# Optimization experiments

Measured on AMD Instinct MI355X. Metric: run time of the kernel, lower is better.

The kernel has to match this reference:

```python
import jax, jax.numpy as jnp
import numpy as np

B, P, D, H, A, C = 256, 512, 16, 256, 8, 2
HID = 256
IN_MLP = H + A + 1  # 265


def setup_inputs() -> dict:
    key = jax.random.key(0)
    ks = jax.random.split(key, 12)
    s = 0.05  # small init for recurrent stability
    return {
        "particles": jax.random.normal(ks[0], (B, P, D), jnp.float32),
        "weights": jax.random.uniform(ks[1], (B, P), jnp.float32),
        "actions": jax.random.normal(ks[2], (B, A), jnp.float32),
        "time": jax.random.uniform(ks[3], (B,), jnp.float32) * 100.0,
        "Wi": jax.random.normal(ks[4], (D + 1, 3 * H), jnp.float32) * s,
        "bi": jnp.zeros((3 * H,), jnp.float32),
        "Wh_rz": jax.random.normal(ks[5], (H, 2 * H), jnp.float32) * s,
        "Wh_n": jax.random.normal(ks[6], (H, H), jnp.float32) * s,
        "bn": jnp.zeros((H,), jnp.float32),
        "mlp_W1": jax.random.normal(ks[7], (C, IN_MLP, HID), jnp.float32) * s,
        "mlp_b1": jnp.zeros((C, HID), jnp.float32),
        "mlp_W2": jax.random.normal(ks[8], (C, HID, HID), jnp.float32) * s,
        "mlp_b2": jnp.zeros((C, HID), jnp.float32),
        "mlp_W3": jax.random.normal(ks[9], (C, HID, 1), jnp.float32) * s,
        "mlp_b3": jnp.zeros((C, 1), jnp.float32),
        "num_time_steps": 100,
    }


def reference(particles, weights, actions, time, Wi, bi, Wh_rz, Wh_n, bn,
              mlp_W1, mlp_b1, mlp_W2, mlp_b2, mlp_W3, mlp_b3, num_time_steps):
    # feature_fn = identity; append weights as an extra feature channel
    x = jnp.concatenate([particles, weights[..., None]], axis=-1)  # [B, P, D+1]
    xs = jnp.swapaxes(x, 0, 1)  # [P, B, D+1], scan over particle axis

    def gru_step(h, xt):
        gi = xt @ Wi + bi  # [B, 3H]
        i_r, i_z, i_n = jnp.split(gi, 3, axis=-1)
        hrz = h @ Wh_rz  # [B, 2H], no bias (flax GRUCell hidden r/z dense)
        r = jax.nn.sigmoid(i_r + hrz[:, :H])
        z = jax.nn.sigmoid(i_z + hrz[:, H:])
        n = jnp.tanh(i_n + r * (h @ Wh_n + bn))
        h_new = (1.0 - z) * n + z * h
        return h_new, None

    h0 = jnp.zeros((particles.shape[0], H), particles.dtype)
    enc, _ = jax.lax.scan(gru_step, h0, xs)  # last hidden == take(outputs, -1, axis=-2)

    norm_time = time / num_time_steps
    hidden = jnp.concatenate([enc, actions, norm_time[..., None]], axis=-1)  # [B, IN_MLP]

    # n_critics MLPs evaluated batched over critic axis c
    h1 = jax.nn.relu(jnp.einsum('bi,cio->bco', hidden, mlp_W1) + mlp_b1)
    h2 = jax.nn.relu(jnp.einsum('bci,cio->bco', h1, mlp_W2) + mlp_b2)
    q = jnp.einsum('bci,cio->bco', h2, mlp_W3) + mlp_b3  # [B, C, 1]
    return q[..., 0]  # [B, C]
```

## Files before the change

kernel.cpp:

```cpp
#include <hip/hip_runtime.h>
#include <hip/hip_fp16.h>

typedef _Float16 h2v __attribute__((ext_vector_type(2)));
typedef _Float16 f16x8 __attribute__((ext_vector_type(8)));
typedef float f32x4 __attribute__((ext_vector_type(4)));
typedef unsigned int u32;
typedef unsigned short u16;

#define NB 256
#define NP 512
#define NH 256

#define OFF_WH 0
#define LEN_WH 98304
#define OFF_WIB (OFF_WH + LEN_WH)
#define LEN_WIB 12288
#define OFF_W1 (OFF_WIB + LEN_WIB)
#define LEN_W1 68096
#define OFF_W2 (OFF_W1 + LEN_W1)
#define LEN_W2 65536
#define OFF_W3 (OFF_W2 + LEN_W2)
#define LEN_W3 256
#define WS_DWORDS (OFF_W3 + LEN_W3)

__device__ __forceinline__ u32 pack2(float lo, float hi) {
    h2v v; v.x = (_Float16)lo; v.y = (_Float16)hi;
    return __builtin_bit_cast(u32, v);
}

__device__ __forceinline__ float fdot2(u32 a, u32 b, float c) {
#if __has_builtin(__builtin_amdgcn_fdot2)
    return __builtin_amdgcn_fdot2(__builtin_bit_cast(h2v, a),
                                  __builtin_bit_cast(h2v, b), c, false);
#else
    h2v x = __builtin_bit_cast(h2v, a), y = __builtin_bit_cast(h2v, b);
    return c + (float)x.x * (float)y.x + (float)x.y * (float)y.y;
#endif
}

__global__ __launch_bounds__(256) void pack_kernel(
    const float* __restrict__ Wi, const float* __restrict__ Whrz,
    const float* __restrict__ Whn, const float* __restrict__ W1,
    const float* __restrict__ W2, const float* __restrict__ W3,
    u32* __restrict__ ws)
{
    for (int F = blockIdx.x * 256 + threadIdx.x; F < WS_DWORDS; F += gridDim.x * 256) {
        u32 val;
        if (F < OFF_WIB) {
            int d = F & 3; int r = F >> 2;
            int l = r & 63; int q = r >> 6;
            int f = q % 48; int w = q / 48;
            int t = f >> 3; int kt = f & 7;
            int g = t >> 1, c = t & 1;
            int k = kt * 32 + ((l >> 4) << 3) + 2 * d;
            int col = g * 256 + w * 32 + c * 16 + (l & 15);
            float lo, hi;
            if (col < 512) { lo = Whrz[k * 512 + col]; hi = Whrz[(k + 1) * 512 + col]; }
            else { lo = Whn[k * 256 + (col - 512)]; hi = Whn[(k + 1) * 256 + (col - 512)]; }
            val = pack2(lo, hi);
        } else if (F < OFF_W1) {
            int j = F - OFF_WIB;
            int d = j & 3; int r = j >> 2;
            int l = r & 63; int q = r >> 6;
            int t = q % 6; int w = q / 6;
            int g = t >> 1, c = t & 1;
            int k = ((l >> 4) << 3) + 2 * d;
            int col = g * 256 + w * 32 + c * 16 + (l & 15);
            float lo = (k < 17) ? Wi[k * 768 + col] : 0.f;
            float hi = (k + 1 < 17) ? Wi[(k + 1) * 768 + col] : 0.f;
            val = pack2(lo, hi);
        } else if (F < OFF_W2) {
            int j = F - OFF_W1; int c = j / (133 * 256); int r = j % (133 * 256);
            int kk = r >> 8; int o = r & 255;
            int k = 2 * kk;
            float lo = W1[(c * 265 + k) * 256 + o];
            float hi = (k + 1 < 265) ? W1[(c * 265 + k + 1) * 256 + o] : 0.f;
            val = pack2(lo, hi);
        } else if (F < OFF_W3) {
            int j = F - OFF_W2; int c = j >> 15; int r = j & 32767;
            int kk = r >> 8; int o = r & 255;
            float lo = W2[(c * 256 + 2 * kk) * 256 + o];
            float hi = W2[(c * 256 + 2 * kk + 1) * 256 + o];
            val = pack2(lo, hi);
        } else {
            int j = F - OFF_W3; int c = j >> 7; int jj = j & 127;
            float lo = W3[c * 256 + 2 * jj];
            float hi = W3[c * 256 + 2 * jj + 1];
            val = pack2(lo, hi);
        }
        ws[F] = val;
    }
}

__global__ __launch_bounds__(512, 2) void qnet_kernel(
    const float* __restrict__ particles, const float* __restrict__ pweights,
    const float* __restrict__ actions, const float* __restrict__ timev,
    const float* __restrict__ bi, const float* __restrict__ bn,
    const float* __restrict__ b1, const float* __restrict__ b2,
    const float* __restrict__ b3, const int* __restrict__ nts,
    const u32* __restrict__ ws, float* __restrict__ out)
{
    __shared__ __align__(16) u32 sX[NP * 16];
    __shared__ __align__(16) float sG[8 * 1536];
    __shared__ __align__(16) u32 sH2[2][128];
    __shared__ __align__(16) float sHf[NH];
    __shared__ __align__(16) float sMisc[16];

    const int b = blockIdx.x;
    const int tid = threadIdx.x;
    const int lane = tid & 63;
    const int wid = tid >> 6;

    f16x8 bfh[48];
    {
        const uint4* gp = (const uint4*)(ws + OFF_WH) + (wid * 48) * 64 + lane;
        #pragma unroll
        for (int i = 0; i < 48; ++i) bfh[i] = __builtin_bit_cast(f16x8, gp[i * 64]);
    }
    {
        const float2* pr2 = (const float2*)(particles + (long)b * NP * 16);
        for (int j = tid; j < NP * 8; j += 512) {
            int p = j >> 3, q = j & 7;
            float2 v = pr2[j];
            sX[p * 16 + q] = pack2(v.x, v.y);
        }
        const float* wr = pweights + (long)b * NP;
        for (int j = tid; j < NP * 8; j += 512) {
            int p = j >> 3, q = j & 7;
            sX[p * 16 + 8 + q] = (q == 0) ? pack2(wr[p], 0.f) : 0u;
        }
    }
    if (tid < 256) ((u32*)sH2)[tid] = 0u;
    if (tid < 8) sMisc[tid] = actions[b * 8 + tid];
    if (tid == 8) sMisc[8] = timev[b] / (float)nts[0];

    float birL = 0.f, bizL = 0.f, binnL = 0.f, bnnL = 0.f, hreg = 0.f;
    if (lane < 32) {
        int j = wid * 32 + lane;
        birL = bi[j]; bizL = bi[NH + j]; binnL = bi[2 * NH + j]; bnnL = bn[j];
    }
    __syncthreads();

    const uint4* wibp = (const uint4*)(ws + OFF_WIB) + (wid * 6) * 64 + lane;

    #pragma unroll 1
    for (int p = 0; p < NP; ++p) {
        if ((p & 15) == 0) {
            f16x8 av = __builtin_bit_cast(f16x8,
                ((const uint4*)sX)[(p + (lane & 15)) * 4 + (lane >> 4)]);
            f32x4 z4 = {0.f, 0.f, 0.f, 0.f};
            f32x4 g0 = __builtin_amdgcn_mfma_f32_16x16x32_f16(av, __builtin_bit_cast(f16x8, wibp[0 * 64]), z4, 0, 0, 0);
            f32x4 g1 = __builtin_amdgcn_mfma_f32_16x16x32_f16(av, __builtin_bit_cast(f16x8, wibp[1 * 64]), z4, 0, 0, 0);
            f32x4 g2 = __builtin_amdgcn_mfma_f32_16x16x32_f16(av, __builtin_bit_cast(f16x8, wibp[2 * 64]), z4, 0, 0, 0);
            f32x4 g3 = __builtin_amdgcn_mfma_f32_16x16x32_f16(av, __builtin_bit_cast(f16x8, wibp[3 * 64]), z4, 0, 0, 0);
            f32x4 g4 = __builtin_amdgcn_mfma_f32_16x16x32_f16(av, __builtin_bit_cast(f16x8, wibp[4 * 64]), z4, 0, 0, 0);
            f32x4 g5 = __builtin_amdgcn_mfma_f32_16x16x32_f16(av, __builtin_bit_cast(f16x8, wibp[5 * 64]), z4, 0, 0, 0);
            int sb = (lane >> 4) << 2;
            float* gw = sG + wid * 1536 + (lane & 15);
            #pragma unroll
            for (int r = 0; r < 4; ++r) {
                gw[(sb + r) * 32]          = g0[r];
                gw[(sb + r) * 32 + 16]     = g1[r];
                gw[512 + (sb + r) * 32]    = g2[r];
                gw[512 + (sb + r) * 32 + 16] = g3[r];
                gw[1024 + (sb + r) * 32]   = g4[r];
                gw[1024 + (sb + r) * 32 + 16] = g5[r];
            }
            __syncthreads();
        }

        float gR = 0.f, gZ = 0.f, gN = 0.f;
        {
            const float* gp = sG + wid * 1536 + (p & 15) * 32 + (lane & 31);
            gR = gp[0]; gZ = gp[512]; gN = gp[1024];
        }

        const u32* hbuf = sH2[p & 1];
        f32x4 a0 = {0.f, 0.f, 0.f, 0.f}, a1 = a0, a2 = a0, a3 = a0, a4 = a0, a5 = a0;
        #pragma unroll
        for (int kt = 0; kt < 8; ++kt) {
            f16x8 hv = __builtin_bit_cast(f16x8, ((const uint4*)hbuf)[kt * 4 + (lane >> 4)]);
            a0 = __builtin_amdgcn_mfma_f32_16x16x32_f16(hv, bfh[kt],      a0, 0, 0, 0);
            a1 = __builtin_amdgcn_mfma_f32_16x16x32_f16(hv, bfh[8 + kt],  a1, 0, 0, 0);
            a2 = __builtin_amdgcn_mfma_f32_16x16x32_f16(hv, bfh[16 + kt], a2, 0, 0, 0);
            a3 = __builtin_amdgcn_mfma_f32_16x16x32_f16(hv, bfh[24 + kt], a3, 0, 0, 0);
            a4 = __builtin_amdgcn_mfma_f32_16x16x32_f16(hv, bfh[32 + kt], a4, 0, 0, 0);
            a5 = __builtin_amdgcn_mfma_f32_16x16x32_f16(hv, bfh[40 + kt], a5, 0, 0, 0);
        }

        bool hic = (lane & 16) != 0;
        float srm = hic ? a1[0] : a0[0];
        float szm = hic ? a3[0] : a2[0];
        float snm = hic ? a5[0] : a4[0];
        if (lane < 32) {
            float xr = gR + birL + srm;
            float xz = gZ + bizL + szm;
            float xn = gN + binnL;
            float r = 1.f / (1.f + __expf(-xr));
            float z = 1.f / (1.f + __expf(-xz));
            float targ = xn + r * (snm + bnnL);
            float e2 = __expf(2.f * targ);
            float n = 1.f - 2.f / (e2 + 1.f);
            hreg = (1.f - z) * n + z * hreg;
            _Float16 hh = (_Float16)hreg;
            ((u16*)sH2[(p + 1) & 1])[wid * 32 + lane] = __builtin_bit_cast(u16, hh);
        }
        __syncthreads();
    }

    if (lane < 32) sHf[wid * 32 + lane] = hreg;
    __syncthreads();
    u32* sHid = (u32*)sG;
    u16* sL1 = (u16*)(sG + 512);
    u16* sL2 = (u16*)(sG + 1024);
    if (tid < 128) sHid[tid] = pack2(sHf[2 * tid], sHf[2 * tid + 1]);
    else if (tid < 132) { int i = tid - 128; sHid[tid] = pack2(sMisc[2 * i], sMisc[2 * i + 1]); }
    else if (tid == 132) sHid[132] = pack2(sMisc[8], 0.f);
    __syncthreads();
    {
        int c = tid >> 8, o = tid & 255;
        float acc = b1[c * 256 + o];
        const u32* wp = ws + OFF_W1 + c * 133 * 256 + o;
        #pragma unroll 4
        for (int kk = 0; kk < 133; ++kk) acc = fdot2(wp[kk * 256], sHid[kk], acc);
        acc = fmaxf(acc, 0.f);
        _Float16 a16 = (_Float16)acc;
        sL1[tid] = __builtin_bit_cast(u16, a16);
    }
    __syncthreads();
    {
        int c = tid >> 8, o = tid & 255;
        float acc = b2[c * 256 + o];
        const u32* wp = ws + OFF_W2 + c * 128 * 256 + o;
        const u32* hp = (const u32*)sL1 + c * 128;
        #pragma unroll 4
        for (int kk = 0; kk < 128; ++kk) acc = fdot2(wp[kk * 256], hp[kk], acc);
        acc = fmaxf(acc, 0.f);
        _Float16 a16 = (_Float16)acc;
        sL2[tid] = __builtin_bit_cast(u16, a16);
    }
    __syncthreads();
    if (tid < 128) {
        int c = tid >> 6, l = tid & 63;
        const u32* wp = ws + OFF_W3 + c * 128;
        const u32* hp = (const u32*)sL2 + c * 128;
        float acc = fdot2(wp[l], hp[l], 0.f);
        acc = fdot2(wp[64 + l], hp[64 + l], acc);
        #pragma unroll
        for (int off = 32; off > 0; off >>= 1) acc += __shfl_down(acc, off);
        if (l == 0) out[b * 2 + c] = acc + b3[c];
    }
}

extern "C" void kernel_launch(void* const* d_in, const int* in_sizes, int n_in,
                              void* d_out, int out_size, void* d_ws, size_t ws_size,
                              hipStream_t stream) {
    const float* particles = (const float*)d_in[0];
    const float* pweights  = (const float*)d_in[1];
    const float* actions   = (const float*)d_in[2];
    const float* timev     = (const float*)d_in[3];
    const float* Wi        = (const float*)d_in[4];
    const float* bi        = (const float*)d_in[5];
    const float* Whrz      = (const float*)d_in[6];
    const float* Whn       = (const float*)d_in[7];
    const float* bn        = (const float*)d_in[8];
    const float* W1        = (const float*)d_in[9];
    const float* b1        = (const float*)d_in[10];
    const float* W2        = (const float*)d_in[11];
    const float* b2        = (const float*)d_in[12];
    const float* W3        = (const float*)d_in[13];
    const float* b3        = (const float*)d_in[14];
    const int*   nts       = (const int*)d_in[15];
    u32* ws = (u32*)d_ws;
    float* outp = (float*)d_out;

    pack_kernel<<<(WS_DWORDS + 255) / 256, 256, 0, stream>>>(Wi, Whrz, Whn, W1, W2, W3, ws);
    qnet_kernel<<<NB, 512, 0, stream>>>(particles, pweights, actions, timev,
                                        bi, bn, b1, b2, b3, nts, ws, outp);
}
```

Measured before the change: 629.6 us.

## Replace per-step MFMA recurrent matvec with packed fp16 dot2 on register-held weights

The recurrent h·Wh product per particle step used MFMA with a 16-row batch where only one row was meaningful, wasting most of the matrix work. It now uses v_dot2 fp16 instructions: each lane holds 192 packed weight pairs for one output column and half of K, and the two halves are reduced with a cross-lane shuffle. The pack kernel is rewritten to produce the new weight layout. This removes the wasted MFMA work but adds more scalar VALU instructions, a shuffle and broadcast LDS reads of h, and raises register pressure to 192 weight registers per lane under launch bounds of 512 threads and 2 blocks, which may cause spills.

Result: slower. 742.9 us (+18.0%).

```diff
diff --git a/kernel.cpp b/kernel.cpp
--- a/kernel.cpp
+++ b/kernel.cpp
@@ -47,13 +47,11 @@
     for (int F = blockIdx.x * 256 + threadIdx.x; F < WS_DWORDS; F += gridDim.x * 256) {
         u32 val;
         if (F < OFF_WIB) {
-            int d = F & 3; int r = F >> 2;
-            int l = r & 63; int q = r >> 6;
-            int f = q % 48; int w = q / 48;
-            int t = f >> 3; int kt = f & 7;
-            int g = t >> 1, c = t & 1;
-            int k = kt * 32 + ((l >> 4) << 3) + 2 * d;
-            int col = g * 256 + w * 32 + c * 16 + (l & 15);
+            int l = F & 63; int t = F >> 6;
+            int i = t % 192; int w = t / 192;
+            int g = i >> 6; int tt = i & 63;
+            int col = g * 256 + w * 32 + (l & 31);
+            int k = ((l >> 5) << 7) + 2 * tt;
             float lo, hi;
             if (col < 512) { lo = Whrz[k * 512 + col]; hi = Whrz[(k + 1) * 512 + col]; }
             else { lo = Whn[k * 256 + (col - 512)]; hi = Whn[(k + 1) * 256 + (col - 512)]; }
@@ -102,7 +100,7 @@
 {
     __shared__ __align__(16) u32 sX[NP * 16];
     __shared__ __align__(16) float sG[8 * 1536];
-    __shared__ __align__(16) u32 sH2[2][128];
+    __shared__ __align__(16) u16 sH2[2][NH];
     __shared__ __align__(16) float sHf[NH];
     __shared__ __align__(16) float sMisc[16];
 
@@ -111,11 +109,11 @@
     const int lane = tid & 63;
     const int wid = tid >> 6;
 
-    f16x8 bfh[48];
-    {
-        const uint4* gp = (const uint4*)(ws + OFF_WH) + (wid * 48) * 64 + lane;
+    u32 wreg[192];
+    {
+        const u32* gp = ws + OFF_WH + (wid * 192) * 64 + lane;
         #pragma unroll
-        for (int i = 0; i < 48; ++i) bfh[i] = __builtin_bit_cast(f16x8, gp[i * 64]);
+        for (int i = 0; i < 192; ++i) wreg[i] = gp[i * 64];
     }
     {
         const float2* pr2 = (const float2*)(particles + (long)b * NP * 16);
@@ -149,61 +147,75 @@
             f16x8 av = __builtin_bit_cast(f16x8,
                 ((const uint4*)sX)[(p + (lane & 15)) * 4 + (lane >> 4)]);
             f32x4 z4 = {0.f, 0.f, 0.f, 0.f};
-            f32x4 g0 = __builtin_amdgcn_mfma_f32_16x16x32_f16(av, __builtin_bit_cast(f16x8, wibp[0 * 64]), z4, 0, 0, 0);
-            f32x4 g1 = __builtin_amdgcn_mfma_f32_16x16x32_f16(av, __builtin_bit_cast(f16x8, wibp[1 * 64]), z4, 0, 0, 0);
-            f32x4 g2 = __builtin_amdgcn_mfma_f32_16x16x32_f16(av, __builtin_bit_cast(f16x8, wibp[2 * 64]), z4, 0, 0, 0);
-            f32x4 g3 = __builtin_amdgcn_mfma_f32_16x16x32_f16(av, __builtin_bit_cast(f16x8, wibp[3 * 64]), z4, 0, 0, 0);
-            f32x4 g4 = __builtin_amdgcn_mfma_f32_16x16x32_f16(av, __builtin_bit_cast(f16x8, wibp[4 * 64]), z4, 0, 0, 0);
-            f32x4 g5 = __builtin_amdgcn_mfma_f32_16x16x32_f16(av, __builtin_bit_cast(f16x8, wibp[5 * 64]), z4, 0, 0, 0);
             int sb = (lane >> 4) << 2;
             float* gw = sG + wid * 1536 + (lane & 15);
-            #pragma unroll
-            for (int r = 0; r < 4; ++r) {
-                gw[(sb + r) * 32]          = g0[r];
-                gw[(sb + r) * 32 + 16]     = g1[r];
-                gw[512 + (sb + r) * 32]    = g2[r];
-                gw[512 + (sb + r) * 32 + 16] = g3[r];
-                gw[1024 + (sb + r) * 32]   = g4[r];
-                gw[1024 + (sb + r) * 32 + 16] = g5[r];
+            {
+                f32x4 g0 = __builtin_amdgcn_mfma_f32_16x16x32_f16(av, __builtin_bit_cast(f16x8, wibp[0 * 64]), z4, 0, 0, 0);
+                f32x4 g1 = __builtin_amdgcn_mfma_f32_16x16x32_f16(av, __builtin_bit_cast(f16x8, wibp[1 * 64]), z4, 0, 0, 0);
+                #pragma unroll
+                for (int r = 0; r < 4; ++r) {
+                    gw[(sb + r) * 32]      = g0[r];
+                    gw[(sb + r) * 32 + 16] = g1[r];
+                }
+            }
+            {
+                f32x4 g2 = __builtin_amdgcn_mfma_f32_16x16x32_f16(av, __builtin_bit_cast(f16x8, wibp[2 * 64]), z4, 0, 0, 0);
+                f32x4 g3 = __builtin_amdgcn_mfma_f32_16x16x32_f16(av, __builtin_bit_cast(f16x8, wibp[3 * 64]), z4, 0, 0, 0);
+                #pragma unroll
+                for (int r = 0; r < 4; ++r) {
+                    gw[512 + (sb + r) * 32]      = g2[r];
+                    gw[512 + (sb + r) * 32 + 16] = g3[r];
+                }
+            }
+            {
+                f32x4 g4 = __builtin_amdgcn_mfma_f32_16x16x32_f16(av, __builtin_bit_cast(f16x8, wibp[4 * 64]), z4, 0, 0, 0);
+                f32x4 g5 = __builtin_amdgcn_mfma_f32_16x16x32_f16(av, __builtin_bit_cast(f16x8, wibp[5 * 64]), z4, 0, 0, 0);
+                #pragma unroll
+                for (int r = 0; r < 4; ++r) {
+                    gw[1024 + (sb + r) * 32]      = g4[r];
+                    gw[1024 + (sb + r) * 32 + 16] = g5[r];
+                }
             }
             __syncthreads();
         }
 
-        float gR = 0.f, gZ = 0.f, gN = 0.f;
+        float gR, gZ, gN;
         {
             const float* gp = sG + wid * 1536 + (p & 15) * 32 + (lane & 31);
             gR = gp[0]; gZ = gp[512]; gN = gp[1024];
         }
 
-        const u32* hbuf = sH2[p & 1];
-        f32x4 a0 = {0.f, 0.f, 0.f, 0.f}, a1 = a0, a2 = a0, a3 = a0, a4 = a0, a5 = a0;
+        const u32* hsrc = (const u32*)(&sH2[p & 1][0]) + ((lane >> 5) << 6);
+        float aR = 0.f, aZ = 0.f, aN = 0.f;
         #pragma unroll
-        for (int kt = 0; kt < 8; ++kt) {
-            f16x8 hv = __builtin_bit_cast(f16x8, ((const uint4*)hbuf)[kt * 4 + (lane >> 4)]);
-            a0 = __builtin_amdgcn_mfma_f32_16x16x32_f16(hv, bfh[kt],      a0, 0, 0, 0);
-            a1 = __builtin_amdgcn_mfma_f32_16x16x32_f16(hv, bfh[8 + kt],  a1, 0, 0, 0);
-            a2 = __builtin_amdgcn_mfma_f32_16x16x32_f16(hv, bfh[16 + kt], a2, 0, 0, 0);
-            a3 = __builtin_amdgcn_mfma_f32_16x16x32_f16(hv, bfh[24 + kt], a3, 0, 0, 0);
-            a4 = __builtin_amdgcn_mfma_f32_16x16x32_f16(hv, bfh[32 + kt], a4, 0, 0, 0);
-            a5 = __builtin_amdgcn_mfma_f32_16x16x32_f16(hv, bfh[40 + kt], a5, 0, 0, 0);
-        }
-
-        bool hic = (lane & 16) != 0;
-        float srm = hic ? a1[0] : a0[0];
-        float szm = hic ? a3[0] : a2[0];
-        float snm = hic ? a5[0] : a4[0];
+        for (int c = 0; c < 8; ++c) {
+            uint4 h0 = ((const uint4*)hsrc)[2 * c];
+            uint4 h1 = ((const uint4*)hsrc)[2 * c + 1];
+            u32 hv[8] = {h0.x, h0.y, h0.z, h0.w, h1.x, h1.y, h1.z, h1.w};
+            #pragma unroll
+            for (int j = 0; j < 8; ++j) {
+                int i = c * 8 + j;
+                aR = fdot2(wreg[i],       hv[j], aR);
+                aZ = fdot2(wreg[64 + i],  hv[j], aZ);
+                aN = fdot2(wreg[128 + i], hv[j], aN);
+            }
+        }
+        aR += __shfl_xor(aR, 32);
+        aZ += __shfl_xor(aZ, 32);
+        aN += __shfl_xor(aN, 32);
+
         if (lane < 32) {
-            float xr = gR + birL + srm;
-            float xz = gZ + bizL + szm;
+            float xr = gR + birL + aR;
+            float xz = gZ + bizL + aZ;
             float xn = gN + binnL;
             float r = 1.f / (1.f + __expf(-xr));
             float z = 1.f / (1.f + __expf(-xz));
-            float targ = xn + r * (snm + bnnL);
+            float targ = xn + r * (aN + bnnL);
             float e2 = __expf(2.f * targ);
             float n = 1.f - 2.f / (e2 + 1.f);
             hreg = (1.f - z) * n + z * hreg;
             _Float16 hh = (_Float16)hreg;
-            ((u16*)sH2[(p + 1) & 1])[wid * 32 + lane] = __builtin_bit_cast(u16, hh);
+            sH2[(p + 1) & 1][wid * 32 + lane] = __builtin_bit_cast(u16, hh);
         }
         __syncthreads();
     }
```
